# Optimization experiments

Hardware: AMD Instinct MI355X
Metric: run time of the kernel (lower is better)

## Reference

```python
import jax, jax.numpy as jnp
import numpy as np

N, N1, N2, E, DIN, H = 100000, 60000, 30000, 1600000, 128, 64


def setup_inputs() -> dict:
    key = jax.random.key(0)
    ks = jax.random.split(key, 16)
    s = 0.05
    return {
        "feats0": jax.random.normal(ks[0], (N, DIN), jnp.float32),
        "feats1": jax.random.normal(ks[1], (N1, DIN), jnp.float32),
        "feats2": jax.random.normal(ks[2], (N2, DIN), jnp.float32),
        "mask_feat": jax.random.normal(ks[3], (N, DIN), jnp.float32),
        "src1": jax.random.randint(ks[4], (E,), 0, N, jnp.int32),
        "dst1": jax.random.randint(ks[5], (E,), 0, N1, jnp.int32),
        "src2": jax.random.randint(ks[6], (E,), 0, N, jnp.int32),
        "dst2": jax.random.randint(ks[7], (E,), 0, N2, jnp.int32),
        "W0": jax.random.normal(ks[8], (DIN, H), jnp.float32) * s,
        "b0": jnp.zeros((H,), jnp.float32),
        "W1": jax.random.normal(ks[9], (DIN, H), jnp.float32) * s,
        "b1": jnp.zeros((H,), jnp.float32),
        "W2": jax.random.normal(ks[10], (DIN, H), jnp.float32) * s,
        "b2": jnp.zeros((H,), jnp.float32),
        "A0": jax.random.normal(ks[11], (H, H), jnp.float32) * s,
        "A1": jax.random.normal(ks[12], (H, H), jnp.float32) * s,
    }


def _mean_agg(h_nei, src, dst, num_tar):
    # sparse mm(nei_index, h_nei) / count  ==  degree-normalized neighbor mean
    summed = jax.ops.segment_sum(h_nei[dst], src, num_segments=num_tar)
    cnt = jax.ops.segment_sum(jnp.ones(src.shape, h_nei.dtype), src, num_segments=num_tar)
    cnt = jnp.where(cnt > 0, cnt, 1.0)[:, None]  # torch.where(count>0, count, 1)
    return summed / cnt


def reference(feats0, feats1, feats2, mask_feat, src1, dst1, src2, dst2,
              W0, b0, W1, b1, W2, b2, A0, A1):
    elu = jax.nn.elu
    h_tar = elu(feats0 @ W0 + b0)
    h_mask = elu(mask_feat @ W0 + b0)
    h_nei1 = elu(feats1 @ W1 + b1)
    h_nei2 = elu(feats2 @ W2 + b2)

    agg1 = _mean_agg(h_nei1, src1, dst1, feats0.shape[0]) @ A0
    agg2 = _mean_agg(h_nei2, src2, dst2, feats0.shape[0]) @ A1

    view1 = elu(h_tar + agg1)
    mask1 = elu(h_mask + agg1)
    view2 = elu(h_tar + agg2)
    mask2 = elu(h_mask + agg2)
    # [5, N, H]: per-relation view/mask embeddings plus coarse target embedding
    return jnp.stack([view1, mask1, view2, mask2, h_tar])
```

## Files before the change

### kernel.cpp

```cpp
#include <hip/hip_runtime.h>
#include <hip/hip_bf16.h>


typedef short  bf16x8 __attribute__((ext_vector_type(8)));
typedef float  f32x4  __attribute__((ext_vector_type(4)));
typedef int    i32x4  __attribute__((ext_vector_type(4)));

#define MFMA_BF16(a, b, c) __builtin_amdgcn_mfma_f32_16x16x32_bf16((a), (b), (c), 0, 0, 0)

__device__ __forceinline__ ushort f2bf(float f) {
  return (ushort)((__float_as_uint(f) + 0x8000u) >> 16);
}
__device__ __forceinline__ float eluf(float x) {
  return x > 0.f ? x : (__expf(x) - 1.f);
}
__device__ __forceinline__ float bflo(unsigned u) { return __uint_as_float(u << 16); }
__device__ __forceinline__ float bfhi(unsigned u) { return __uint_as_float(u & 0xFFFF0000u); }
__device__ __forceinline__ bf16x8 cvt8(const float* __restrict__ p) {
  f32x4 lo = *(const f32x4*)p;
  f32x4 hi = *(const f32x4*)(p + 4);
  union { unsigned u[4]; bf16x8 v; } r;
#pragma unroll
  for (int j = 0; j < 2; ++j) {
    unsigned a = __float_as_uint(lo[2 * j])     + 0x8000u;
    unsigned b = __float_as_uint(lo[2 * j + 1]) + 0x8000u;
    r.u[j] = (a >> 16) | (b & 0xFFFF0000u);
    unsigned c = __float_as_uint(hi[2 * j])     + 0x8000u;
    unsigned d = __float_as_uint(hi[2 * j + 1]) + 0x8000u;
    r.u[2 + j] = (c >> 16) | (d & 0xFFFF0000u);
  }
  return r.v;
}

__global__ __launch_bounds__(256) void pack_frags_kernel(
    const float* __restrict__ W0, const float* __restrict__ W1,
    const float* __restrict__ W2, const float* __restrict__ A0,
    const float* __restrict__ A1, ushort* __restrict__ out) {
  int gw   = (blockIdx.x * blockDim.x + threadIdx.x) >> 6;
  int lane = threadIdx.x & 63;
  if (gw >= 64) return;
  const float* src; ushort* dst; int f;
  if (gw < 16)      { src = W0; dst = out;         f = gw;      }
  else if (gw < 32) { src = W1; dst = out + 8192;  f = gw - 16; }
  else if (gw < 48) { src = W2; dst = out + 16384; f = gw - 32; }
  else if (gw < 56) { src = A0; dst = out + 24576; f = gw - 48; }
  else              { src = A1; dst = out + 28672; f = gw - 56; }
  int kc = f >> 2, ct = f & 3;
  int q = lane >> 4, c = lane & 15;
  ushort* d = dst + ((size_t)f * 64 + lane) * 8;
#pragma unroll
  for (int i = 0; i < 8; ++i)
    d[i] = f2bf(src[(kc * 32 + q * 8 + i) * 64 + ct * 16 + c]);
}

template <bool HASA>
__global__ __launch_bounds__(256) void lin_elu_kernel(
    const float* __restrict__ X, const ushort* __restrict__ Wp,
    const float* __restrict__ bias, const ushort* __restrict__ Ap,
    void* __restrict__ Yv, int Mtiles) {
  __shared__ ushort plds[4][16 * 72];
  int lane  = threadIdx.x & 63;
  int q     = lane >> 4, c = lane & 15;
  int wslot = threadIdx.x >> 6;
  int wid   = blockIdx.x * 4 + wslot;
  int nw    = gridDim.x * 4;

  bf16x8 bw[4][4];
#pragma unroll
  for (int kc = 0; kc < 4; ++kc)
#pragma unroll
    for (int ct = 0; ct < 4; ++ct)
      bw[kc][ct] = *(const bf16x8*)(Wp + (((kc << 2) | ct) * 64 + lane) * 8);

  float bv[4];
#pragma unroll
  for (int ct = 0; ct < 4; ++ct) bv[ct] = bias[ct * 16 + c];

  bf16x8 ba[2][4];
  if (HASA) {
#pragma unroll
    for (int kc = 0; kc < 2; ++kc)
#pragma unroll
      for (int ct = 0; ct < 4; ++ct)
        ba[kc][ct] = *(const bf16x8*)(Ap + (((kc << 2) | ct) * 64 + lane) * 8);
  }

  ushort* myp = plds[wslot];

  for (int t = wid; t < Mtiles; t += nw) {
    const float* xr = X + ((size_t)(t * 16 + c)) * 128 + q * 8;
    bf16x8 a0 = cvt8(xr);
    bf16x8 a1 = cvt8(xr + 32);
    bf16x8 a2 = cvt8(xr + 64);
    bf16x8 a3 = cvt8(xr + 96);

    f32x4 acc[4];
#pragma unroll
    for (int ct = 0; ct < 4; ++ct) {
      f32x4 a = {0.f, 0.f, 0.f, 0.f};
      a = MFMA_BF16(a0, bw[0][ct], a);
      a = MFMA_BF16(a1, bw[1][ct], a);
      a = MFMA_BF16(a2, bw[2][ct], a);
      a = MFMA_BF16(a3, bw[3][ct], a);
      acc[ct] = a;
    }

    if (!HASA) {
      float* yr = (float*)Yv + ((size_t)t * 16) * 64;
#pragma unroll
      for (int ct = 0; ct < 4; ++ct)
#pragma unroll
        for (int r = 0; r < 4; ++r)
          yr[(q * 4 + r) * 64 + ct * 16 + c] = eluf(acc[ct][r] + bv[ct]);
    } else {
#pragma unroll
      for (int ct = 0; ct < 4; ++ct)
#pragma unroll
        for (int r = 0; r < 4; ++r)
          myp[(q * 4 + r) * 72 + ct * 16 + c] = f2bf(eluf(acc[ct][r] + bv[ct]));
      bf16x8 p0 = *(const bf16x8*)(myp + c * 72 + q * 8);
      bf16x8 p1 = *(const bf16x8*)(myp + c * 72 + 32 + q * 8);
      f32x4 acc2[4];
#pragma unroll
      for (int ct = 0; ct < 4; ++ct) {
        f32x4 a = {0.f, 0.f, 0.f, 0.f};
        a = MFMA_BF16(p0, ba[0][ct], a);
        a = MFMA_BF16(p1, ba[1][ct], a);
        acc2[ct] = a;
      }
      ushort* yb = (ushort*)Yv + ((size_t)t * 16) * 64;
#pragma unroll
      for (int ct = 0; ct < 4; ++ct)
#pragma unroll
        for (int r = 0; r < 4; ++r)
          yb[(q * 4 + r) * 64 + ct * 16 + c] = f2bf(acc2[ct][r]);
    }
  }
}

__global__ __launch_bounds__(256) void bucket_count_kernel(
    const int* __restrict__ src1, const int* __restrict__ src2,
    int* __restrict__ btot, int E, int N) {
  __shared__ int h[256];
  int t = threadIdx.x;
  h[t] = 0;
  __syncthreads();
  int n4 = (2 * E) >> 2;
  int stride = gridDim.x * blockDim.x;
  for (int i = blockIdx.x * blockDim.x + t; i < n4; i += stride) {
    int e4 = i << 2;
    i32x4 k;
    if (e4 < E) k = *(const i32x4*)(src1 + e4);
    else {
      k = *(const i32x4*)(src2 + (e4 - E));
#pragma unroll
      for (int j = 0; j < 4; ++j) k[j] += N;
    }
#pragma unroll
    for (int j = 0; j < 4; ++j) atomicAdd(&h[k[j] >> 10], 1);
  }
  __syncthreads();
  if (h[t]) atomicAdd(&btot[t], h[t]);
}

__global__ __launch_bounds__(256) void bscan_kernel(
    const int* __restrict__ btot, int* __restrict__ bstart,
    int* __restrict__ bcur, int NB) {
  __shared__ int lds[256];
  int t = threadIdx.x;
  int v = (t < NB) ? btot[t] : 0;
  lds[t] = v; __syncthreads();
  for (int off = 1; off < 256; off <<= 1) {
    int x = lds[t];
    int a = (t >= off) ? lds[t - off] : 0;
    __syncthreads();
    lds[t] = x + a;
    __syncthreads();
  }
  int incl = lds[t];
  if (t < NB) { bstart[t] = incl - v; bcur[t] = incl - v; }
  if (t == NB - 1) bstart[NB] = incl;
}

#define P1_CHUNK 8192
__global__ __launch_bounds__(256) void partition_kernel(
    const int* __restrict__ src1, const int* __restrict__ dst1,
    const int* __restrict__ src2, const int* __restrict__ dst2,
    int* __restrict__ bcur, unsigned* __restrict__ pairs, int E, int N) {
  __shared__ int hist[256], sbuf[256], lbase[256], lcur[256], gstart[256];
  __shared__ unsigned img[P1_CHUNK];
  int t  = threadIdx.x;
  int M  = 2 * N;
  int NB = (M + 1023) >> 10;
  int cb = blockIdx.x * P1_CHUNK;
  int ng = (2 * E - cb) >> 2;
  if (ng > P1_CHUNK / 4) ng = P1_CHUNK / 4;

  hist[t] = 0;
  __syncthreads();

  for (int i = t; i < ng; i += 256) {
    int e4 = cb + (i << 2);
    i32x4 k;
    if (e4 < E) k = *(const i32x4*)(src1 + e4);
    else {
      k = *(const i32x4*)(src2 + (e4 - E));
#pragma unroll
      for (int j = 0; j < 4; ++j) k[j] += N;
    }
#pragma unroll
    for (int j = 0; j < 4; ++j) atomicAdd(&hist[k[j] >> 10], 1);
  }
  __syncthreads();

  sbuf[t] = hist[t];
  __syncthreads();
  for (int off = 1; off < 256; off <<= 1) {
    int x = sbuf[t];
    int a = (t >= off) ? sbuf[t - off] : 0;
    __syncthreads();
    sbuf[t] = x + a;
    __syncthreads();
  }
  lbase[t] = sbuf[t] - hist[t];
  lcur[t]  = sbuf[t] - hist[t];
  if (t < NB) gstart[t] = atomicAdd(&bcur[t], hist[t]);
  __syncthreads();

  for (int i = t; i < ng; i += 256) {
    int e4 = cb + (i << 2);
    i32x4 k, v;
    if (e4 < E) {
      k = *(const i32x4*)(src1 + e4);
      v = *(const i32x4*)(dst1 + e4);
    } else {
      k = *(const i32x4*)(src2 + (e4 - E));
      v = *(const i32x4*)(dst2 + (e4 - E));
#pragma unroll
      for (int j = 0; j < 4; ++j) k[j] += N;
    }
#pragma unroll
    for (int j = 0; j < 4; ++j) {
      int b  = k[j] >> 10;
      int lp = atomicAdd(&lcur[b], 1);
      img[lp] = ((unsigned)(k[j] & 1023) << 16) | (unsigned)v[j];
    }
  }
  __syncthreads();

  int w = t >> 6, lane = t & 63;
  for (int b = w; b < NB; b += 4) {
    int len = hist[b], lb = lbase[b], gs = gstart[b];
    for (int i = lane; i < len; i += 64)
      pairs[gs + i] = img[lb + i];
  }
}

#define P2_CAP 18432
__global__ __launch_bounds__(256) void scatter_kernel(
    const int* __restrict__ bstart, const unsigned* __restrict__ pairs,
    int* __restrict__ row_ptr, int* __restrict__ nbr, int M) {
  __shared__ int cur[1024];
  __shared__ int ssum[256];
  __shared__ int img[P2_CAP];
  int t     = threadIdx.x;
  int b     = blockIdx.x;
  int kbase = b << 10;
  int kend  = kbase + 1024; if (kend > M) kend = M;
  int kcnt  = kend - kbase;
  int pbase = bstart[b];
  int cnt   = bstart[b + 1] - pbase;

#pragma unroll
  for (int j = 0; j < 4; ++j) cur[t * 4 + j] = 0;
  __syncthreads();
  for (int i = t; i < cnt; i += 256)
    atomicAdd(&cur[pairs[pbase + i] >> 16], 1);
  __syncthreads();

  int c0 = cur[t * 4], c1 = cur[t * 4 + 1], c2 = cur[t * 4 + 2], c3 = cur[t * 4 + 3];
  int s  = c0 + c1 + c2 + c3;
  ssum[t] = s;
  __syncthreads();
  for (int off = 1; off < 256; off <<= 1) {
    int x = ssum[t];
    int a = (t >= off) ? ssum[t - off] : 0;
    __syncthreads();
    ssum[t] = x + a;
    __syncthreads();
  }
  int run = ssum[t] - s;
  int e0 = run, e1 = run + c0, e2 = e1 + c1, e3 = e2 + c2;
  cur[t * 4] = e0; cur[t * 4 + 1] = e1; cur[t * 4 + 2] = e2; cur[t * 4 + 3] = e3;
  if (t * 4 + 3 < kcnt) {
    i32x4 rp = { pbase + e0, pbase + e1, pbase + e2, pbase + e3 };
    *(i32x4*)(row_ptr + kbase + t * 4) = rp;
  } else {
    if (t * 4     < kcnt) row_ptr[kbase + t * 4]     = pbase + e0;
    if (t * 4 + 1 < kcnt) row_ptr[kbase + t * 4 + 1] = pbase + e1;
    if (t * 4 + 2 < kcnt) row_ptr[kbase + t * 4 + 2] = pbase + e2;
    if (t * 4 + 3 < kcnt) row_ptr[kbase + t * 4 + 3] = pbase + e3;
  }
  if (t == 0 && kend == M) row_ptr[M] = pbase + cnt;
  __syncthreads();

  for (int i = t; i < cnt; i += 256) {
    unsigned p = pairs[pbase + i];
    int kl = (int)(p >> 16);
    int v  = (int)(p & 0xFFFFu);
    int pos = atomicAdd(&cur[kl], 1);
    if (pos < P2_CAP) img[pos] = v;
    else              nbr[pbase + pos] = v;
  }
  __syncthreads();

  int lim = cnt < P2_CAP ? cnt : P2_CAP;
  for (int i = t; i < lim; i += 256) nbr[pbase + i] = img[i];
}

__global__ __launch_bounds__(256) void aggregate_kernel(
    const int* __restrict__ row_ptr, const int* __restrict__ nbr,
    const ushort* __restrict__ g1, const ushort* __restrict__ g2,
    ushort* __restrict__ avg1, ushort* __restrict__ avg2, int N) {
  int lane = threadIdx.x & 63;
  int v = blockIdx.x * 4 + (threadIdx.x >> 6);
  if (v >= 2 * N) return;
  int n0 = row_ptr[v], n1 = row_ptr[v + 1];
  const ushort* __restrict__ g = (v < N) ? g1 : g2;
  int half = lane >> 5;
  int c2   = (lane & 31) << 1;
  float ax = 0.f, ay = 0.f;
  for (int base = n0; base < n1; base += 64) {
    int rem = n1 - base;
    int m = rem < 64 ? rem : 64;
    int idx = (lane < m) ? nbr[base + lane] : 0;
    int j = 0;
    for (; j + 8 <= m; j += 8) {
      int d0 = __shfl(idx, j + half);
      int d1 = __shfl(idx, j + 2 + half);
      int d2 = __shfl(idx, j + 4 + half);
      int d3 = __shfl(idx, j + 6 + half);
      unsigned u0 = *(const unsigned*)(g + (size_t)d0 * 64 + c2);
      unsigned u1 = *(const unsigned*)(g + (size_t)d1 * 64 + c2);
      unsigned u2 = *(const unsigned*)(g + (size_t)d2 * 64 + c2);
      unsigned u3 = *(const unsigned*)(g + (size_t)d3 * 64 + c2);
      ax += bflo(u0) + bflo(u1) + bflo(u2) + bflo(u3);
      ay += bfhi(u0) + bfhi(u1) + bfhi(u2) + bfhi(u3);
    }
    for (; j < m; j += 2) {
      int jj = j + half;
      int d = __shfl(idx, jj);
      unsigned u = *(const unsigned*)(g + (size_t)d * 64 + c2);
      if (jj < m) { ax += bflo(u); ay += bfhi(u); }
    }
  }
  ax += __shfl_xor(ax, 32);
  ay += __shfl_xor(ay, 32);
  if (lane < 32) {
    int deg = n1 - n0;
    float s = (deg > 0) ? 1.f / (float)deg : 0.f;
    unsigned w = (unsigned)f2bf(ax * s) | ((unsigned)f2bf(ay * s) << 16);
    ushort* av = (v < N) ? avg1 : avg2;
    int vv = (v < N) ? v : v - N;
    *(unsigned*)(av + (size_t)vv * 64 + c2) = w;
  }
}

__global__ __launch_bounds__(256) void finalize_kernel(
    const ushort* __restrict__ avg1, const ushort* __restrict__ avg2,
    float* __restrict__ out, int N) {
  int i = blockIdx.x * blockDim.x + threadIdx.x;
  if (i >= N * 16) return;
  size_t base  = ((size_t)i) << 2;
  size_t plane = (size_t)N * 64;
  f32x4 t = *(const f32x4*)(out + 4 * plane + base);
  f32x4 m = *(const f32x4*)(out + plane + base);
  unsigned a1l = *(const unsigned*)(avg1 + base);
  unsigned a1h = *(const unsigned*)(avg1 + base + 2);
  unsigned a2l = *(const unsigned*)(avg2 + base);
  unsigned a2h = *(const unsigned*)(avg2 + base + 2);
  float a1[4] = { bflo(a1l), bfhi(a1l), bflo(a1h), bfhi(a1h) };
  float a2[4] = { bflo(a2l), bfhi(a2l), bflo(a2h), bfhi(a2h) };
  f32x4 v1, m1, v2, m2;
#pragma unroll
  for (int j = 0; j < 4; ++j) {
    v1[j] = eluf(t[j] + a1[j]);
    m1[j] = eluf(m[j] + a1[j]);
    v2[j] = eluf(t[j] + a2[j]);
    m2[j] = eluf(m[j] + a2[j]);
  }
  *(f32x4*)(out + base)             = v1;
  *(f32x4*)(out + plane + base)     = m1;
  *(f32x4*)(out + 2 * plane + base) = v2;
  *(f32x4*)(out + 3 * plane + base) = m2;
}

static inline int imin(int a, int b) { return a < b ? a : b; }

extern "C" void kernel_launch(void* const* d_in, const int* in_sizes, int n_in,
                              void* d_out, int out_size, void* d_ws, size_t ws_size,
                              hipStream_t stream) {
  const float* feats0 = (const float*)d_in[0];
  const float* feats1 = (const float*)d_in[1];
  const float* feats2 = (const float*)d_in[2];
  const float* maskf  = (const float*)d_in[3];
  const int* src1 = (const int*)d_in[4];
  const int* dst1 = (const int*)d_in[5];
  const int* src2 = (const int*)d_in[6];
  const int* dst2 = (const int*)d_in[7];
  const float* W0 = (const float*)d_in[8];
  const float* b0 = (const float*)d_in[9];
  const float* W1 = (const float*)d_in[10];
  const float* b1 = (const float*)d_in[11];
  const float* W2 = (const float*)d_in[12];
  const float* b2 = (const float*)d_in[13];
  const float* A0 = (const float*)d_in[14];
  const float* A1 = (const float*)d_in[15];

  int N  = in_sizes[0] / 128;
  int N1 = in_sizes[1] / 128;
  int N2 = in_sizes[2] / 128;
  int E  = in_sizes[4];
  int M  = 2 * N;

  float* out = (float*)d_out;
  size_t plane = (size_t)N * 64;
  float* h_tar  = out + 4 * plane;
  float* h_mask = out + plane;

  ushort* frags  = (ushort*)d_ws;
  int* row_ptr   = (int*)((char*)d_ws + 65536);
  int* btot      = row_ptr + M + 1;
  int* bstart    = btot + 256;
  int* bcur      = bstart + 257;
  int* nbr       = bcur + 256;
  unsigned* pairs = (unsigned*)(nbr + 2 * E);
  ushort* g1b    = (ushort*)(pairs + 2 * E);
  ushort* g2b    = g1b + (size_t)N1 * 64;
  ushort* avg1b  = g2b + (size_t)N2 * 64;
  ushort* avg2b  = avg1b + (size_t)N * 64;

  hipMemsetAsync(btot, 0, 256 * sizeof(int), stream);

  pack_frags_kernel<<<16, 256, 0, stream>>>(W0, W1, W2, A0, A1, frags);

  int t0 = N / 16, t1 = N1 / 16, t2 = N2 / 16;
  lin_elu_kernel<false><<<imin(2048, (t0 + 3) / 4), 256, 0, stream>>>(
      feats0, frags, b0, nullptr, h_tar, t0);
  lin_elu_kernel<false><<<imin(2048, (t0 + 3) / 4), 256, 0, stream>>>(
      maskf, frags, b0, nullptr, h_mask, t0);
  lin_elu_kernel<true><<<imin(2048, (t1 + 3) / 4), 256, 0, stream>>>(
      feats1, frags + 8192, b1, frags + 24576, g1b, t1);
  lin_elu_kernel<true><<<imin(2048, (t2 + 3) / 4), 256, 0, stream>>>(
      feats2, frags + 16384, b2, frags + 28672, g2b, t2);

  int NB = (M + 1023) >> 10;
  bucket_count_kernel<<<512, 256, 0, stream>>>(src1, src2, btot, E, N);
  bscan_kernel<<<1, 256, 0, stream>>>(btot, bstart, bcur, NB);

  int p1blocks = (2 * E + P1_CHUNK - 1) / P1_CHUNK;
  partition_kernel<<<p1blocks, 256, 0, stream>>>(
      src1, dst1, src2, dst2, bcur, pairs, E, N);
  scatter_kernel<<<NB, 256, 0, stream>>>(bstart, pairs, row_ptr, nbr, M);

  aggregate_kernel<<<(M + 3) / 4, 256, 0, stream>>>(
      row_ptr, nbr, g1b, g2b, avg1b, avg2b, N);

  finalize_kernel<<<(N * 16 + 255) / 256, 256, 0, stream>>>(avg1b, avg2b, out, N);
}
```

Measured before the change: 484.1 us.

## Fuse neighbor aggregation with final ELU epilogue and widen gather loads

Merges the aggregate and finalize kernels into one. Each wavefront now handles one target node across both relations and applies the ELU combine directly, so the bf16 avg1/avg2 intermediates and their global round trip go away. The gather switches from 4-byte per-lane loads (2 neighbors per step) to 16-byte loads (8 neighbors per step), with a 3-step shuffle reduction and shared memory to redistribute the sums. Workspace is reordered so the gathered g1/g2 buffers sit near the front. This adds per-wave work and drops the rounding of the averages to bf16.

After: 456.6 us. 5.7% less time.

```diff
diff --git a/kernel.cpp b/kernel.cpp
--- a/kernel.cpp
+++ b/kernel.cpp
@@ -5,6 +5,7 @@
 typedef short  bf16x8 __attribute__((ext_vector_type(8)));
 typedef float  f32x4  __attribute__((ext_vector_type(4)));
 typedef int    i32x4  __attribute__((ext_vector_type(4)));
+typedef unsigned u32x4 __attribute__((ext_vector_type(4)));
 
 #define MFMA_BF16(a, b, c) __builtin_amdgcn_mfma_f32_16x16x32_bf16((a), (b), (c), 0, 0, 0)
 
@@ -318,81 +319,91 @@
   for (int i = t; i < lim; i += 256) nbr[pbase + i] = img[i];
 }
 
-__global__ __launch_bounds__(256) void aggregate_kernel(
+__global__ __launch_bounds__(256) void agg_final_kernel(
     const int* __restrict__ row_ptr, const int* __restrict__ nbr,
     const ushort* __restrict__ g1, const ushort* __restrict__ g2,
-    ushort* __restrict__ avg1, ushort* __restrict__ avg2, int N) {
-  int lane = threadIdx.x & 63;
-  int v = blockIdx.x * 4 + (threadIdx.x >> 6);
-  if (v >= 2 * N) return;
-  int n0 = row_ptr[v], n1 = row_ptr[v + 1];
-  const ushort* __restrict__ g = (v < N) ? g1 : g2;
-  int half = lane >> 5;
-  int c2   = (lane & 31) << 1;
-  float ax = 0.f, ay = 0.f;
-  for (int base = n0; base < n1; base += 64) {
-    int rem = n1 - base;
-    int m = rem < 64 ? rem : 64;
-    int idx = (lane < m) ? nbr[base + lane] : 0;
-    int j = 0;
-    for (; j + 8 <= m; j += 8) {
-      int d0 = __shfl(idx, j + half);
-      int d1 = __shfl(idx, j + 2 + half);
-      int d2 = __shfl(idx, j + 4 + half);
-      int d3 = __shfl(idx, j + 6 + half);
-      unsigned u0 = *(const unsigned*)(g + (size_t)d0 * 64 + c2);
-      unsigned u1 = *(const unsigned*)(g + (size_t)d1 * 64 + c2);
-      unsigned u2 = *(const unsigned*)(g + (size_t)d2 * 64 + c2);
-      unsigned u3 = *(const unsigned*)(g + (size_t)d3 * 64 + c2);
-      ax += bflo(u0) + bflo(u1) + bflo(u2) + bflo(u3);
-      ay += bfhi(u0) + bfhi(u1) + bfhi(u2) + bfhi(u3);
-    }
-    for (; j < m; j += 2) {
-      int jj = j + half;
-      int d = __shfl(idx, jj);
-      unsigned u = *(const unsigned*)(g + (size_t)d * 64 + c2);
-      if (jj < m) { ax += bflo(u); ay += bfhi(u); }
-    }
-  }
-  ax += __shfl_xor(ax, 32);
-  ay += __shfl_xor(ay, 32);
-  if (lane < 32) {
+    float* __restrict__ out, int N) {
+  __shared__ float sh[4][2][64];
+  int lane  = threadIdx.x & 63;
+  int wslot = threadIdx.x >> 6;
+  int v = blockIdx.x * 4 + wslot;
+  if (v >= N) return;
+  int e8  = lane >> 3;
+  int lgo = (lane & 7) << 4;
+
+#pragma unroll
+  for (int r = 0; r < 2; ++r) {
+    int key = v + r * N;
+    int n0 = row_ptr[key], n1 = row_ptr[key + 1];
+    const char* gb = (const char*)(r ? g2 : g1);
+    float acc[8];
+#pragma unroll
+    for (int c = 0; c < 8; ++c) acc[c] = 0.f;
+
+    for (int base = n0; base < n1; base += 64) {
+      int m = n1 - base; if (m > 64) m = 64;
+      int idx = (lane < m) ? nbr[base + lane] : 0;
+      int j = 0;
+      for (; j + 16 <= m; j += 16) {
+        int d0 = __shfl(idx, j + e8);
+        int d1 = __shfl(idx, j + 8 + e8);
+        u32x4 u0 = *(const u32x4*)(gb + (unsigned)((d0 << 7) + lgo));
+        u32x4 u1 = *(const u32x4*)(gb + (unsigned)((d1 << 7) + lgo));
+#pragma unroll
+        for (int c = 0; c < 4; ++c) {
+          acc[2 * c]     += bflo(u0[c]) + bflo(u1[c]);
+          acc[2 * c + 1] += bfhi(u0[c]) + bfhi(u1[c]);
+        }
+      }
+      if (j + 8 <= m) {
+        int d0 = __shfl(idx, j + e8);
+        u32x4 u0 = *(const u32x4*)(gb + (unsigned)((d0 << 7) + lgo));
+#pragma unroll
+        for (int c = 0; c < 4; ++c) {
+          acc[2 * c]     += bflo(u0[c]);
+          acc[2 * c + 1] += bfhi(u0[c]);
+        }
+        j += 8;
+      }
+      if (j < m) {
+        int jj = j + e8;
+        int d0 = __shfl(idx, jj & 63);
+        u32x4 u0 = *(const u32x4*)(gb + (unsigned)((d0 << 7) + lgo));
+        if (jj < m) {
+#pragma unroll
+          for (int c = 0; c < 4; ++c) {
+            acc[2 * c]     += bflo(u0[c]);
+            acc[2 * c + 1] += bfhi(u0[c]);
+          }
+        }
+      }
+    }
+
+#pragma unroll
+    for (int c = 0; c < 8; ++c) {
+      acc[c] += __shfl_xor(acc[c], 8);
+      acc[c] += __shfl_xor(acc[c], 16);
+      acc[c] += __shfl_xor(acc[c], 32);
+    }
     int deg = n1 - n0;
     float s = (deg > 0) ? 1.f / (float)deg : 0.f;
-    unsigned w = (unsigned)f2bf(ax * s) | ((unsigned)f2bf(ay * s) << 16);
-    ushort* av = (v < N) ? avg1 : avg2;
-    int vv = (v < N) ? v : v - N;
-    *(unsigned*)(av + (size_t)vv * 64 + c2) = w;
-  }
-}
-
-__global__ __launch_bounds__(256) void finalize_kernel(
-    const ushort* __restrict__ avg1, const ushort* __restrict__ avg2,
-    float* __restrict__ out, int N) {
-  int i = blockIdx.x * blockDim.x + threadIdx.x;
-  if (i >= N * 16) return;
-  size_t base  = ((size_t)i) << 2;
+    if (lane < 8) {
+      float* dp = &sh[wslot][r][lane * 8];
+#pragma unroll
+      for (int c = 0; c < 8; ++c) dp[c] = acc[c] * s;
+    }
+  }
+
+  float a1 = sh[wslot][0][lane];
+  float a2 = sh[wslot][1][lane];
   size_t plane = (size_t)N * 64;
-  f32x4 t = *(const f32x4*)(out + 4 * plane + base);
-  f32x4 m = *(const f32x4*)(out + plane + base);
-  unsigned a1l = *(const unsigned*)(avg1 + base);
-  unsigned a1h = *(const unsigned*)(avg1 + base + 2);
-  unsigned a2l = *(const unsigned*)(avg2 + base);
-  unsigned a2h = *(const unsigned*)(avg2 + base + 2);
-  float a1[4] = { bflo(a1l), bfhi(a1l), bflo(a1h), bfhi(a1h) };
-  float a2[4] = { bflo(a2l), bfhi(a2l), bflo(a2h), bfhi(a2h) };
-  f32x4 v1, m1, v2, m2;
-#pragma unroll
-  for (int j = 0; j < 4; ++j) {
-    v1[j] = eluf(t[j] + a1[j]);
-    m1[j] = eluf(m[j] + a1[j]);
-    v2[j] = eluf(t[j] + a2[j]);
-    m2[j] = eluf(m[j] + a2[j]);
-  }
-  *(f32x4*)(out + base)             = v1;
-  *(f32x4*)(out + plane + base)     = m1;
-  *(f32x4*)(out + 2 * plane + base) = v2;
-  *(f32x4*)(out + 3 * plane + base) = m2;
+  size_t o = (size_t)v * 64 + lane;
+  float t  = out[4 * plane + o];
+  float mm = out[plane + o];
+  out[o]             = eluf(t + a1);
+  out[plane + o]     = eluf(mm + a1);
+  out[2 * plane + o] = eluf(t + a2);
+  out[3 * plane + o] = eluf(mm + a2);
 }
 
 static inline int imin(int a, int b) { return a < b ? a : b; }
@@ -429,16 +440,14 @@
   float* h_mask = out + plane;
 
   ushort* frags  = (ushort*)d_ws;
-  int* row_ptr   = (int*)((char*)d_ws + 65536);
+  ushort* g1b    = frags + 32768;
+  ushort* g2b    = g1b + (size_t)N1 * 64;
+  int* row_ptr   = (int*)(g2b + (size_t)N2 * 64);
   int* btot      = row_ptr + M + 1;
   int* bstart    = btot + 256;
   int* bcur      = bstart + 257;
-  int* nbr       = bcur + 256;
+  int* nbr       = bcur + 258;
   unsigned* pairs = (unsigned*)(nbr + 2 * E);
-  ushort* g1b    = (ushort*)(pairs + 2 * E);
-  ushort* g2b    = g1b + (size_t)N1 * 64;
-  ushort* avg1b  = g2b + (size_t)N2 * 64;
-  ushort* avg2b  = avg1b + (size_t)N * 64;
 
   hipMemsetAsync(btot, 0, 256 * sizeof(int), stream);
 
@@ -463,8 +472,6 @@
       src1, dst1, src2, dst2, bcur, pairs, E, N);
   scatter_kernel<<<NB, 256, 0, stream>>>(bstart, pairs, row_ptr, nbr, M);
 
-  aggregate_kernel<<<(M + 3) / 4, 256, 0, stream>>>(
-      row_ptr, nbr, g1b, g2b, avg1b, avg2b, N);
-
-  finalize_kernel<<<(N * 16 + 255) / 256, 256, 0, stream>>>(avg1b, avg2b, out, N);
-}
+  agg_final_kernel<<<(N + 3) / 4, 256, 0, stream>>>(
+      row_ptr, nbr, g1b, g2b, out, N);
+}
```
